# Kernel optimization log

Measured on AMD Instinct MI355X. Metric: run time of the kernel, lower is better.

## Reference

```python
import jax, jax.numpy as jnp
import numpy as np

N = 50000   # nodes
E = 800000  # directed edges
D = 128     # input_feat_dim
H = 128     # hidden1
L = 3       # GatedGraphConv layers
G = 64      # num graphs in batch
NEG_SLOPE = 0.01


def setup_inputs() -> dict:
    key = jax.random.key(0)
    ks = jax.random.split(key, 12)
    s = 1.0 / np.sqrt(H)
    x = jax.random.normal(ks[0], (N, D), jnp.float32)
    edge_index = jax.random.randint(ks[1], (2, E), 0, N)
    batch = jnp.sort(jax.random.randint(ks[2], (N,), 0, G))
    W_gcn = jax.random.normal(ks[3], (D, H), jnp.float32) * s
    b_gcn = jnp.zeros((H,), jnp.float32)
    W_gg = jax.random.normal(ks[4], (L, H, H), jnp.float32) * s   # GatedGraphConv per-layer weight
    W_ih = jax.random.normal(ks[5], (3 * H, H), jnp.float32) * s  # GRUCell input weights (r,z,n)
    W_hh = jax.random.normal(ks[6], (3 * H, H), jnp.float32) * s  # GRUCell hidden weights
    b_ih = jnp.zeros((3 * H,), jnp.float32)
    b_hh = jnp.zeros((3 * H,), jnp.float32)
    W1 = jax.random.normal(ks[7], (H, H), jnp.float32) * s
    b1 = jnp.zeros((H,), jnp.float32)
    W2 = jax.random.normal(ks[8], (H, 1), jnp.float32) * s
    b2 = jnp.zeros((1,), jnp.float32)
    return dict(x=x, edge_index=edge_index, batch=batch, W_gcn=W_gcn, b_gcn=b_gcn,
                W_gg=W_gg, W_ih=W_ih, W_hh=W_hh, b_ih=b_ih, b_hh=b_hh,
                W1=W1, b1=b1, W2=W2, b2=b2)


def _seg(vals, idx, num):
    return jax.ops.segment_sum(vals, idx, num_segments=num)


def _gcn(x, row, col, W, b):
    # PyG GCNConv: add self loops, symmetric norm, aggregate at target (col)
    xw = x @ W
    deg = _seg(jnp.ones((E,), xw.dtype), col, N) + 1.0  # +1 for self loop
    dinv = jax.lax.rsqrt(deg)
    norm = dinv[row] * dinv[col]                         # [E]
    out = _seg(xw[row] * norm[:, None], col, N)          # gather-scale-scatter
    out = out + xw * (dinv * dinv)[:, None]              # self-loop term
    return out + b


def _gru(m, h, W_ih, W_hh, b_ih, b_hh):
    gi = m @ W_ih.T + b_ih
    gh = h @ W_hh.T + b_hh
    ir, iz, inn = jnp.split(gi, 3, axis=-1)
    hr, hz, hn = jnp.split(gh, 3, axis=-1)
    r = jax.nn.sigmoid(ir + hr)
    z = jax.nn.sigmoid(iz + hz)
    n = jnp.tanh(inn + r * hn)
    return (1.0 - z) * n + z * h


def reference(x, edge_index, batch, W_gcn, b_gcn, W_gg, W_ih, W_hh, b_ih, b_hh, W1, b1, W2, b2):
    row, col = edge_index[0], edge_index[1]
    h = jax.nn.leaky_relu(_gcn(x, row, col, W_gcn, b_gcn), NEG_SLOPE)   # [N,H]
    g = h
    for l in range(L):  # GatedGraphConv: message = x_j @ W_l, sum-aggregate at col, GRU update
        m = _seg((g @ W_gg[l])[row], col, N)
        g = _gru(m, g, W_ih, W_hh, b_ih, b_hh)
    h = jax.nn.leaky_relu(g, NEG_SLOPE) + h
    h = jax.nn.leaky_relu(h @ W1 + b1, NEG_SLOPE)
    probs = jax.nn.sigmoid(h @ W2 + b2)                                  # [N,1]
    # maxcut loss: per-graph expected cut
    degrees = _seg(jnp.ones((E,), probs.dtype), row, N)[:, None]         # degree(row) per node
    expected_weight = _seg(probs[row] * probs[col], batch[row], G)       # [G,1]
    expected_degree = _seg(probs * degrees, batch, G)                    # [G,1]
    return -(expected_degree - expected_weight) / 2.0                    # [G,1]
```

## Files before the change

kernel.cpp:

```cpp
#include <hip/hip_runtime.h>
#include <math.h>

#define HD 128
#define NEG 0.01f
#define GD 64
#define LDST 136
#define FST 132

typedef short bf16x8 __attribute__((ext_vector_type(8)));
typedef float floatx4 __attribute__((ext_vector_type(4)));

__device__ __forceinline__ unsigned short f2bf(float f) {
    unsigned int u = __float_as_uint(f);
    u += 0x7fffu + ((u >> 16) & 1u);
    return (unsigned short)(u >> 16);
}
__device__ __forceinline__ float bf2f(unsigned short b) {
    return __uint_as_float(((unsigned int)b) << 16);
}
__device__ __forceinline__ float sigm(float v) { return 1.f / (1.f + __expf(-v)); }

__device__ __forceinline__ void mm64(const unsigned short* __restrict__ ap,
                                     const unsigned short* __restrict__ W,
                                     int m16, int quad, floatx4* acc) {
    #pragma unroll
    for (int ks = 0; ks < 4; ks++) {
        const int koff = ks * 32 + quad * 8;
        bf16x8 a = *(const bf16x8*)(ap + koff);
        #pragma unroll
        for (int cg = 0; cg < 8; cg++) {
            bf16x8 b = *(const bf16x8*)(W + (size_t)(cg * 16 + m16) * HD + koff);
            acc[cg] = __builtin_amdgcn_mfma_f32_16x16x32_bf16(a, b, acc[cg], 0, 0, 0);
        }
    }
}

__device__ __forceinline__ void loadB(const unsigned short* __restrict__ W,
                                      int w, int m16, int quad, bf16x8 bf[2][4]) {
    #pragma unroll
    for (int cgl = 0; cgl < 2; cgl++)
        #pragma unroll
        for (int ks = 0; ks < 4; ks++)
            bf[cgl][ks] = *(const bf16x8*)(W + (size_t)((2 * w + cgl) * 16 + m16) * HD
                                           + ks * 32 + quad * 8);
}
__device__ __forceinline__ void mmAcc32(const unsigned short* __restrict__ Atile,
                                        int m16, int quad, const bf16x8 bf[2][4],
                                        floatx4 acc[2][2]) {
    #pragma unroll
    for (int rg = 0; rg < 2; rg++)
        #pragma unroll
        for (int ks = 0; ks < 4; ks++) {
            bf16x8 a = *(const bf16x8*)(Atile + (rg * 16 + m16) * LDST + ks * 32 + quad * 8);
            acc[rg][0] = __builtin_amdgcn_mfma_f32_16x16x32_bf16(a, bf[0][ks], acc[rg][0], 0, 0, 0);
            acc[rg][1] = __builtin_amdgcn_mfma_f32_16x16x32_bf16(a, bf[1][ks], acc[rg][1], 0, 0, 0);
        }
}

__global__ __launch_bounds__(256) void gemm_mfma(
    const unsigned short* __restrict__ A, const unsigned short* __restrict__ BT,
    float* __restrict__ C32, unsigned short* __restrict__ C16, int M)
{
    __shared__ unsigned short As[128 * LDST];
    __shared__ unsigned short Bs[128 * LDST];
    const int tid = threadIdx.x;
    const int r0 = blockIdx.x * 128;
    {
        int rowi = tid >> 1, half = tid & 1;
        int gr = r0 + rowi; if (gr >= M) gr = M - 1;
        const float4* sa = (const float4*)(A + (size_t)gr * HD + half * 64);
        float4* da = (float4*)(As + rowi * LDST + half * 64);
        const float4* sb = (const float4*)(BT + (size_t)rowi * HD + half * 64);
        float4* db = (float4*)(Bs + rowi * LDST + half * 64);
        #pragma unroll
        for (int i = 0; i < 8; i++) { da[i] = sa[i]; db[i] = sb[i]; }
    }
    __syncthreads();
    const int wave = tid >> 6, lane = tid & 63;
    const int m16 = lane & 15, quad = lane >> 4;
    floatx4 acc[2][8];
    #pragma unroll
    for (int i = 0; i < 2; i++)
        #pragma unroll
        for (int j = 0; j < 8; j++) acc[i][j] = (floatx4){0.f, 0.f, 0.f, 0.f};
    const unsigned short* ar0 = As + (wave * 32 + m16) * LDST;
    const unsigned short* ar1 = As + (wave * 32 + 16 + m16) * LDST;
    #pragma unroll
    for (int ks = 0; ks < 4; ks++) {
        const int koff = ks * 32 + quad * 8;
        bf16x8 a0 = *(const bf16x8*)(ar0 + koff);
        bf16x8 a1 = *(const bf16x8*)(ar1 + koff);
        #pragma unroll
        for (int cg = 0; cg < 8; cg++) {
            bf16x8 b = *(const bf16x8*)(Bs + (cg * 16 + m16) * LDST + koff);
            acc[0][cg] = __builtin_amdgcn_mfma_f32_16x16x32_bf16(a0, b, acc[0][cg], 0, 0, 0);
            acc[1][cg] = __builtin_amdgcn_mfma_f32_16x16x32_bf16(a1, b, acc[1][cg], 0, 0, 0);
        }
    }
    if (C32) {
        #pragma unroll
        for (int rg = 0; rg < 2; rg++)
            #pragma unroll
            for (int cg = 0; cg < 8; cg++)
                #pragma unroll
                for (int i = 0; i < 4; i++) {
                    int r = r0 + wave * 32 + rg * 16 + quad * 4 + i;
                    if (r < M) C32[(size_t)r * HD + cg * 16 + m16] = acc[rg][cg][i];
                }
    }
    __syncthreads();
    #pragma unroll
    for (int rg = 0; rg < 2; rg++)
        #pragma unroll
        for (int cg = 0; cg < 8; cg++)
            #pragma unroll
            for (int i = 0; i < 4; i++)
                As[(wave * 32 + rg * 16 + quad * 4 + i) * LDST + cg * 16 + m16] =
                    f2bf(acc[rg][cg][i]);
    __syncthreads();
    #pragma unroll
    for (int it = 0; it < 8; it++) {
        int idx = it * 2048 + tid * 8;
        int rowi = idx >> 7, c = idx & 127;
        int gr = r0 + rowi;
        if (gr < M) {
            uint4 v = *(const uint4*)(As + rowi * LDST + c);
            *(uint4*)(C16 + (size_t)gr * HD + c) = v;
        }
    }
}

__global__ __launch_bounds__(256) void k_gather_gcn(
    const unsigned short* __restrict__ src, const float* __restrict__ xw,
    const int* __restrict__ csr, const int* __restrict__ offs,
    const float* __restrict__ dinv, const float* __restrict__ bias,
    float* __restrict__ h, unsigned short* __restrict__ g16, int N)
{
    int node = blockIdx.x * 4 + (threadIdx.x >> 6);
    if (node >= N) return;
    int lane = threadIdx.x & 63;
    int sub = lane >> 4, cl = lane & 15;
    int s = offs[node], e = offs[node + 1];
    float acc[8] = {0.f, 0.f, 0.f, 0.f, 0.f, 0.f, 0.f, 0.f};
    int j = s;
    for (; j + 8 <= e; j += 8) {
        int ra = csr[j + sub], rb = csr[j + 4 + sub];
        float sa = dinv[ra], sb = dinv[rb];
        bf16x8 va = *(const bf16x8*)(src + (size_t)ra * HD + cl * 8);
        bf16x8 vb = *(const bf16x8*)(src + (size_t)rb * HD + cl * 8);
        #pragma unroll
        for (int q = 0; q < 8; q++)
            acc[q] += bf2f((unsigned short)va[q]) * sa + bf2f((unsigned short)vb[q]) * sb;
    }
    for (; j < e; j += 4) {
        int jj = j + sub;
        if (jj < e) {
            int r = csr[jj];
            float sc = dinv[r];
            bf16x8 v = *(const bf16x8*)(src + (size_t)r * HD + cl * 8);
            #pragma unroll
            for (int q = 0; q < 8; q++)
                acc[q] += bf2f((unsigned short)v[q]) * sc;
        }
    }
    #pragma unroll
    for (int q = 0; q < 8; q++) {
        acc[q] += __shfl_xor(acc[q], 16);
        acc[q] += __shfl_xor(acc[q], 32);
    }
    if (sub == 0) {
        float dn = dinv[node], dv2 = dn * dn;
        size_t base = (size_t)node * HD + cl * 8;
        float4 xv0 = *(const float4*)(xw + base);
        float4 xv1 = *(const float4*)(xw + base + 4);
        float xs[8] = {xv0.x, xv0.y, xv0.z, xv0.w, xv1.x, xv1.y, xv1.z, xv1.w};
        float o[8];
        #pragma unroll
        for (int q = 0; q < 8; q++) {
            float v = acc[q] * dn + xs[q] * dv2 + bias[cl * 8 + q];
            o[q] = v > 0.f ? v : v * NEG;
        }
        *(float4*)(h + base) = (float4){o[0], o[1], o[2], o[3]};
        *(float4*)(h + base + 4) = (float4){o[4], o[5], o[6], o[7]};
        uint4 st;
        st.x = (unsigned int)f2bf(o[0]) | ((unsigned int)f2bf(o[1]) << 16);
        st.y = (unsigned int)f2bf(o[2]) | ((unsigned int)f2bf(o[3]) << 16);
        st.z = (unsigned int)f2bf(o[4]) | ((unsigned int)f2bf(o[5]) << 16);
        st.w = (unsigned int)f2bf(o[6]) | ((unsigned int)f2bf(o[7]) << 16);
        *(uint4*)(g16 + base) = st;
    }
}

__global__ __launch_bounds__(256) void k_gather_m(
    const unsigned short* __restrict__ src, const int* __restrict__ csr,
    const int* __restrict__ offs, unsigned short* __restrict__ out16, int N)
{
    int node = blockIdx.x * 4 + (threadIdx.x >> 6);
    if (node >= N) return;
    int lane = threadIdx.x & 63;
    int sub = lane >> 4, cl = lane & 15;
    int s = offs[node], e = offs[node + 1];
    float acc[8] = {0.f, 0.f, 0.f, 0.f, 0.f, 0.f, 0.f, 0.f};
    int j = s;
    for (; j + 8 <= e; j += 8) {
        int ra = csr[j + sub], rb = csr[j + 4 + sub];
        bf16x8 va = *(const bf16x8*)(src + (size_t)ra * HD + cl * 8);
        bf16x8 vb = *(const bf16x8*)(src + (size_t)rb * HD + cl * 8);
        #pragma unroll
        for (int q = 0; q < 8; q++)
            acc[q] += bf2f((unsigned short)va[q]) + bf2f((unsigned short)vb[q]);
    }
    for (; j < e; j += 4) {
        int jj = j + sub;
        if (jj < e) {
            int r = csr[jj];
            bf16x8 v = *(const bf16x8*)(src + (size_t)r * HD + cl * 8);
            #pragma unroll
            for (int q = 0; q < 8; q++)
                acc[q] += bf2f((unsigned short)v[q]);
        }
    }
    #pragma unroll
    for (int q = 0; q < 8; q++) {
        acc[q] += __shfl_xor(acc[q], 16);
        acc[q] += __shfl_xor(acc[q], 32);
    }
    if (sub == 0) {
        uint4 st;
        st.x = (unsigned int)f2bf(acc[0]) | ((unsigned int)f2bf(acc[1]) << 16);
        st.y = (unsigned int)f2bf(acc[2]) | ((unsigned int)f2bf(acc[3]) << 16);
        st.z = (unsigned int)f2bf(acc[4]) | ((unsigned int)f2bf(acc[5]) << 16);
        st.w = (unsigned int)f2bf(acc[6]) | ((unsigned int)f2bf(acc[7]) << 16);
        *(uint4*)(out16 + (size_t)node * HD + cl * 8) = st;
    }
}

__global__ __launch_bounds__(256, 5) void k_gru_gates(
    const unsigned short* __restrict__ m_bf, const unsigned short* __restrict__ g_bf,
    const unsigned short* __restrict__ Wih, const unsigned short* __restrict__ Whh,
    const float* __restrict__ b_ih, const float* __restrict__ b_hh,
    unsigned short* __restrict__ g16_out, int M)
{
    __shared__ unsigned short sh[2 * 32 * LDST];
    unsigned short* Am = sh;
    unsigned short* Ag = sh + 32 * LDST;
    const int tid = threadIdx.x;
    const int r0 = blockIdx.x * 32;
    #pragma unroll
    for (int it = 0; it < 2; it++) {
        int idx = it * 2048 + tid * 8;
        int rowi = idx >> 7, c = idx & 127;
        int gr = r0 + rowi; if (gr >= M) gr = M - 1;
        *(float4*)(Am + rowi * LDST + c) = *(const float4*)(m_bf + (size_t)gr * HD + c);
        *(float4*)(Ag + rowi * LDST + c) = *(const float4*)(g_bf + (size_t)gr * HD + c);
    }
    __syncthreads();
    const int w = tid >> 6, l = tid & 63;
    const int m16 = l & 15, quad = l >> 4;

    floatx4 accA[2][2], accB[2][2];
    bf16x8 bf[2][4];
    #pragma unroll
    for (int rg = 0; rg < 2; rg++)
        #pragma unroll
        for (int c = 0; c < 2; c++) {
            accA[rg][c] = (floatx4){0.f, 0.f, 0.f, 0.f};
            accB[rg][c] = (floatx4){0.f, 0.f, 0.f, 0.f};
        }
    loadB(Wih, w, m16, quad, bf);
    mmAcc32(Am, m16, quad, bf, accA);
    loadB(Whh, w, m16, quad, bf);
    mmAcc32(Ag, m16, quad, bf, accA);
    loadB(Whh + 256 * HD, w, m16, quad, bf);
    mmAcc32(Ag, m16, quad, bf, accB);
    #pragma unroll
    for (int cgl = 0; cgl < 2; cgl++) {
        int c = (2 * w + cgl) * 16 + m16;
        float br = b_ih[c] + b_hh[c];
        float bhn = b_hh[256 + c];
        #pragma unroll
        for (int rg = 0; rg < 2; rg++)
            #pragma unroll
            for (int i = 0; i < 4; i++) {
                float r = sigm(accA[rg][cgl][i] + br);
                accB[rg][cgl][i] = r * (accB[rg][cgl][i] + bhn);
            }
    }
    loadB(Wih + 256 * HD, w, m16, quad, bf);
    mmAcc32(Am, m16, quad, bf, accB);
    #pragma unroll
    for (int rg = 0; rg < 2; rg++)
        #pragma unroll
        for (int c = 0; c < 2; c++) accA[rg][c] = (floatx4){0.f, 0.f, 0.f, 0.f};
    loadB(Wih + 128 * HD, w, m16, quad, bf);
    mmAcc32(Am, m16, quad, bf, accA);
    loadB(Whh + 128 * HD, w, m16, quad, bf);
    mmAcc32(Ag, m16, quad, bf, accA);
    float ov[2][2][4];
    #pragma unroll
    for (int cgl = 0; cgl < 2; cgl++) {
        int c = (2 * w + cgl) * 16 + m16;
        float bz = b_ih[128 + c] + b_hh[128 + c];
        float bin = b_ih[256 + c];
        #pragma unroll
        for (int rg = 0; rg < 2; rg++)
            #pragma unroll
            for (int i = 0; i < 4; i++) {
                float z = sigm(accA[rg][cgl][i] + bz);
                float n = tanhf(accB[rg][cgl][i] + bin);
                float gv = bf2f(Ag[(rg * 16 + quad * 4 + i) * LDST + c]);
                ov[cgl][rg][i] = (1.f - z) * n + z * gv;
            }
    }
    __syncthreads();
    float* shf = (float*)sh;
    #pragma unroll
    for (int cgl = 0; cgl < 2; cgl++) {
        int c = (2 * w + cgl) * 16 + m16;
        #pragma unroll
        for (int rg = 0; rg < 2; rg++)
            #pragma unroll
            for (int i = 0; i < 4; i++)
                shf[(rg * 16 + quad * 4 + i) * FST + c] = ov[cgl][rg][i];
    }
    __syncthreads();
    #pragma unroll
    for (int it = 0; it < 2; it++) {
        int idx = it * 2048 + tid * 8;
        int rowi = idx >> 7, c = idx & 127;
        int gr = r0 + rowi;
        if (gr < M) {
            float4 v0 = *(const float4*)(shf + rowi * FST + c);
            float4 v1 = *(const float4*)(shf + rowi * FST + c + 4);
            uint4 st;
            st.x = (unsigned int)f2bf(v0.x) | ((unsigned int)f2bf(v0.y) << 16);
            st.y = (unsigned int)f2bf(v0.z) | ((unsigned int)f2bf(v0.w) << 16);
            st.z = (unsigned int)f2bf(v1.x) | ((unsigned int)f2bf(v1.y) << 16);
            st.w = (unsigned int)f2bf(v1.z) | ((unsigned int)f2bf(v1.w) << 16);
            *(uint4*)(g16_out + (size_t)gr * HD + c) = st;
        }
    }
}

__global__ __launch_bounds__(256, 4) void k_head_fused(
    const unsigned short* __restrict__ g_bf, const float* __restrict__ h,
    const unsigned short* __restrict__ W1T, const float* __restrict__ b1,
    const float* __restrict__ W2, const float* __restrict__ b2,
    float* __restrict__ probs, int M)
{
    __shared__ unsigned short As[64 * LDST];
    const int tid = threadIdx.x;
    const int r0 = blockIdx.x * 64;
    {
        int rowi = tid >> 2, q = tid & 3;
        int gr = r0 + rowi; if (gr >= M) gr = M - 1;
        const unsigned short* gp = g_bf + (size_t)gr * HD + q * 32;
        const float* hp = h + (size_t)gr * HD + q * 32;
        unsigned short* dst = As + rowi * LDST + q * 32;
        #pragma unroll
        for (int i = 0; i < 32; i += 4) {
            ushort4 gu = *(const ushort4*)(gp + i);
            float4 hv = *(const float4*)(hp + i);
            ushort4 o;
            float v;
            v = bf2f(gu.x); v = v > 0.f ? v : v * NEG; o.x = f2bf(v + hv.x);
            v = bf2f(gu.y); v = v > 0.f ? v : v * NEG; o.y = f2bf(v + hv.y);
            v = bf2f(gu.z); v = v > 0.f ? v : v * NEG; o.z = f2bf(v + hv.z);
            v = bf2f(gu.w); v = v > 0.f ? v : v * NEG; o.w = f2bf(v + hv.w);
            *(ushort4*)(dst + i) = o;
        }
    }
    __syncthreads();
    const int w = tid >> 6, l = tid & 63;
    const int m16 = l & 15, quad = l >> 4;
    floatx4 acc[8];
    #pragma unroll
    for (int j = 0; j < 8; j++) acc[j] = (floatx4){0.f, 0.f, 0.f, 0.f};
    mm64(As + (w * 16 + m16) * LDST, W1T, m16, quad, acc);
    #pragma unroll
    for (int i = 0; i < 4; i++) {
        float s = 0.f;
        #pragma unroll
        for (int cg = 0; cg < 8; cg++) {
            int c = cg * 16 + m16;
            float v = acc[cg][i] + b1[c];
            v = v > 0.f ? v : v * NEG;
            s += v * W2[c];
        }
        s += __shfl_xor(s, 1); s += __shfl_xor(s, 2);
        s += __shfl_xor(s, 4); s += __shfl_xor(s, 8);
        int r = r0 + w * 16 + quad * 4 + i;
        if (m16 == 0 && r < M) probs[r] = sigm(s + b2[0]);
    }
}

__global__ void k_prep_w(const float* __restrict__ W_gcn, const float* __restrict__ W_gg,
                         const float* __restrict__ W_ih, const float* __restrict__ W_hh,
                         const float* __restrict__ W1, unsigned short* __restrict__ Wq) {
    int i = blockIdx.x * blockDim.x + threadIdx.x;
    if (i >= 180224) return;
    float v;
    if (i < 16384) {
        int n = i >> 7, k = i & 127;
        v = W_gcn[k * 128 + n];
    } else if (i < 65536) {
        int j = i - 16384;
        int l = j >> 14, rr = j & 16383;
        int n = rr >> 7, k = rr & 127;
        v = W_gg[l * 16384 + k * 128 + n];
    } else if (i < 114688) {
        v = W_ih[i - 65536];
    } else if (i < 163840) {
        v = W_hh[i - 114688];
    } else {
        int j = i - 163840;
        int n = j >> 7, k = j & 127;
        v = W1[k * 128 + n];
    }
    Wq[i] = f2bf(v);
}

__global__ void k_cast_x(const float* __restrict__ s, unsigned short* __restrict__ d, int n2) {
    int i = blockIdx.x * blockDim.x + threadIdx.x;
    if (i >= n2) return;
    float2 v = *(const float2*)(s + (size_t)i * 2);
    unsigned int p = (unsigned int)f2bf(v.x) | ((unsigned int)f2bf(v.y) << 16);
    *(unsigned int*)(d + (size_t)i * 2) = p;
}

__global__ void k_hist(const int* __restrict__ col, int* __restrict__ cnt4,
                       int* __restrict__ rank, int N, int E) {
    int e = blockIdx.x * blockDim.x + threadIdx.x;
    if (e < E) {
        int s = blockIdx.x & 3;
        rank[e] = atomicAdd(&cnt4[s * N + col[e]], 1);
    }
}

#define SCHUNK 2048
__global__ __launch_bounds__(256) void k_scan1(const int* __restrict__ cnt4,
                                               int* __restrict__ excl,
                                               int* __restrict__ bsum, int N) {
    __shared__ int ts[256];
    int t = threadIdx.x;
    int base = blockIdx.x * SCHUNK + t * 8;
    int v[8]; int s = 0;
    #pragma unroll
    for (int q = 0; q < 8; q++) {
        int i = base + q;
        v[q] = (i < N) ? (cnt4[i] + cnt4[N + i] + cnt4[2 * N + i] + cnt4[3 * N + i]) : 0;
        s += v[q];
    }
    ts[t] = s;
    __syncthreads();
    for (int off = 1; off < 256; off <<= 1) {
        int a = (t >= off) ? ts[t - off] : 0;
        __syncthreads();
        ts[t] += a;
        __syncthreads();
    }
    int run = ts[t] - s;
    #pragma unroll
    for (int q = 0; q < 8; q++) { int i = base + q; if (i < N) excl[i] = run; run += v[q]; }
    if (t == 255) bsum[blockIdx.x] = ts[255];
}

__global__ void k_scan2(int* bsum, int nb) {
    if (threadIdx.x == 0) {
        int run = 0;
        for (int b = 0; b < nb; b++) { int v = bsum[b]; bsum[b] = run; run += v; }
    }
}

__global__ void k_csrfin(const int* __restrict__ excl, const int* __restrict__ bsum,
                         const int* __restrict__ cnt4, int* __restrict__ offs,
                         int* __restrict__ sbase, float* __restrict__ dinv, int N, int E) {
    int i = blockIdx.x * blockDim.x + threadIdx.x;
    if (i >= N) return;
    int o = excl[i] + bsum[i >> 11];
    offs[i] = o;
    if (i == 0) offs[N] = E;
    int c0 = cnt4[i], c1 = cnt4[N + i], c2 = cnt4[2 * N + i], c3 = cnt4[3 * N + i];
    sbase[i] = o;
    sbase[N + i] = o + c0;
    sbase[2 * N + i] = o + c0 + c1;
    sbase[3 * N + i] = o + c0 + c1 + c2;
    dinv[i] = rsqrtf((float)(c0 + c1 + c2 + c3) + 1.f);
}

__global__ void k_fill(const int* __restrict__ row, const int* __restrict__ col,
                       const int* __restrict__ sbase, const int* __restrict__ rank,
                       int* __restrict__ csr_rows, int N, int E) {
    int e = blockIdx.x * blockDim.x + threadIdx.x;
    if (e >= E) return;
    int s = (e >> 8) & 3;
    csr_rows[sbase[s * N + col[e]] + rank[e]] = row[e];
}

__global__ __launch_bounds__(256) void k_loss_edge(const float* __restrict__ probs,
                                                   const int* __restrict__ row,
                                                   const int* __restrict__ col,
                                                   const int* __restrict__ batch,
                                                   float* __restrict__ ed,
                                                   float* __restrict__ ew, int E) {
    __shared__ float bd[GD], be[GD];
    if (threadIdx.x < GD) { bd[threadIdx.x] = 0.f; be[threadIdx.x] = 0.f; }
    __syncthreads();
    for (int e = blockIdx.x * blockDim.x + threadIdx.x; e < E; e += gridDim.x * blockDim.x) {
        int r = row[e];
        float pr = probs[r];
        int b = batch[r];
        atomicAdd(&bd[b], pr);
        atomicAdd(&be[b], pr * probs[col[e]]);
    }
    __syncthreads();
    if (threadIdx.x < GD) {
        atomicAdd(&ed[threadIdx.x], bd[threadIdx.x]);
        atomicAdd(&ew[threadIdx.x], be[threadIdx.x]);
    }
}

__global__ void k_finalize(const float* __restrict__ ed, const float* __restrict__ ew,
                           float* __restrict__ out) {
    int g = threadIdx.x;
    if (g < GD) out[g] = -(ed[g] - ew[g]) * 0.5f;
}

extern "C" void kernel_launch(void* const* d_in, const int* in_sizes, int n_in,
                              void* d_out, int out_size, void* d_ws, size_t ws_size,
                              hipStream_t stream) {
    const float* x     = (const float*)d_in[0];
    const int*   ei    = (const int*)d_in[1];
    const int*   batch = (const int*)d_in[2];
    const float* W_gcn = (const float*)d_in[3];
    const float* b_gcn = (const float*)d_in[4];
    const float* W_gg  = (const float*)d_in[5];
    const float* W_ih  = (const float*)d_in[6];
    const float* W_hh  = (const float*)d_in[7];
    const float* b_ih  = (const float*)d_in[8];
    const float* b_hh  = (const float*)d_in[9];
    const float* W1    = (const float*)d_in[10];
    const float* b1    = (const float*)d_in[11];
    const float* W2    = (const float*)d_in[12];
    const float* b2    = (const float*)d_in[13];
    float* out = (float*)d_out;

    const int N = in_sizes[2];
    const int E = in_sizes[1] / 2;
    const int* row = ei;
    const int* col = ei + E;
    const size_t NH = (size_t)N * HD;

    float* F = (float*)d_ws;
    float* f_h  = F + 0 * NH;
    float* f_xw = F + 1 * NH;
    unsigned short* U = (unsigned short*)(F + 2 * NH);
    unsigned short* x_bf  = U;
    unsigned short* g_bf  = U + 1 * NH;
    unsigned short* t_bf  = U + 2 * NH;
    unsigned short* m_bf  = U + 3 * NH;
    unsigned short* Wq    = U + 4 * NH;
    unsigned short* WgcnT = Wq;
    unsigned short* WggT  = Wq + 16384;
    unsigned short* Wih16 = Wq + 65536;
    unsigned short* Whh16 = Wq + 114688;
    unsigned short* W1T   = Wq + 163840;
    float* S = (float*)(Wq + 180224);
    float* f_dinv  = S;
    float* f_probs = S + N;
    float* f_ed    = S + 2 * N;
    float* f_ew    = f_ed + GD;
    int* I = (int*)(f_ew + GD);
    int* i_cnt4  = I;
    int* i_excl  = I + 4 * N;
    int* i_offs  = I + 5 * N;
    int* i_bsum  = I + 6 * N + 8;
    int* i_sbase = I + 6 * N + 128;
    int* i_rank  = I + 10 * N + 128;
    int* i_csr   = i_rank + E;

    const int nb_scan = (N + SCHUNK - 1) / SCHUNK;
    const int gb32 = (N + 31) / 32;
    const int gb64 = (N + 63) / 64;
    const int gb128 = (N + 127) / 128;
    const int eg = (E + 255) / 256;
    const int ng = (N + 255) / 256;
    const int gather_grid = (N + 3) / 4;

    hipMemsetAsync(i_cnt4, 0, sizeof(int) * 4 * (size_t)N, stream);
    hipMemsetAsync(f_ed, 0, sizeof(float) * 2 * GD, stream);

    k_prep_w<<<704, 256, 0, stream>>>(W_gcn, W_gg, W_ih, W_hh, W1, Wq);
    k_cast_x<<<(int)((NH / 2 + 255) / 256), 256, 0, stream>>>(x, x_bf, (int)(NH / 2));

    k_hist<<<eg, 256, 0, stream>>>(col, i_cnt4, i_rank, N, E);
    k_scan1<<<nb_scan, 256, 0, stream>>>(i_cnt4, i_excl, i_bsum, N);
    k_scan2<<<1, 64, 0, stream>>>(i_bsum, nb_scan);
    k_csrfin<<<ng, 256, 0, stream>>>(i_excl, i_bsum, i_cnt4, i_offs, i_sbase, f_dinv, N, E);
    k_fill<<<eg, 256, 0, stream>>>(row, col, i_sbase, i_rank, i_csr, N, E);

    gemm_mfma<<<gb128, 256, 0, stream>>>(x_bf, WgcnT, f_xw, t_bf, N);
    k_gather_gcn<<<gather_grid, 256, 0, stream>>>(t_bf, f_xw, i_csr, i_offs, f_dinv,
                                                  b_gcn, f_h, g_bf, N);

    for (int l = 0; l < 3; l++) {
        gemm_mfma<<<gb128, 256, 0, stream>>>(g_bf, WggT + (size_t)l * 16384,
                                             nullptr, t_bf, N);
        k_gather_m<<<gather_grid, 256, 0, stream>>>(t_bf, i_csr, i_offs, m_bf, N);
        k_gru_gates<<<gb32, 256, 0, stream>>>(m_bf, g_bf, Wih16, Whh16, b_ih, b_hh,
                                              g_bf, N);
    }

    k_head_fused<<<gb64, 256, 0, stream>>>(g_bf, f_h, W1T, b1, W2, b2, f_probs, N);

    k_loss_edge<<<1024, 256, 0, stream>>>(f_probs, row, col, batch, f_ed, f_ew, E);
    k_finalize<<<1, 64, 0, stream>>>(f_ed, f_ew, out);
}
```

Baseline: 586.6 us.

## Double-buffer GRU weight loads, use exp-based tanh, widen histogram sharding to 8

Inside the GRU gate kernel, the next weight fragments are now loaded into a second register buffer while the current MFMA block runs, so global-load latency can overlap with matrix work. tanhf is replaced by an exp-based formula to cut transcendental cost. The CSR-build histogram spreads its atomic counters over 8 shards instead of 4 to reduce atomic contention, at the cost of more scan and finalize memory traffic. The extra register buffer may increase register pressure and lower occupancy.

New measurement: 574.2 us. -2.1%, faster.

```diff
diff --git a/kernel.cpp b/kernel.cpp
--- a/kernel.cpp
+++ b/kernel.cpp
@@ -19,6 +19,7 @@
     return __uint_as_float(((unsigned int)b) << 16);
 }
 __device__ __forceinline__ float sigm(float v) { return 1.f / (1.f + __expf(-v)); }
+__device__ __forceinline__ float fast_tanh(float v) { return 2.f / (1.f + __expf(-2.f * v)) - 1.f; }
 
 __device__ __forceinline__ void mm64(const unsigned short* __restrict__ ap,
                                      const unsigned short* __restrict__ W,
@@ -259,7 +260,7 @@
     const int m16 = l & 15, quad = l >> 4;
 
     floatx4 accA[2][2], accB[2][2];
-    bf16x8 bf[2][4];
+    bf16x8 bfA[2][4], bfB[2][4];
     #pragma unroll
     for (int rg = 0; rg < 2; rg++)
         #pragma unroll
@@ -267,12 +268,13 @@
             accA[rg][c] = (floatx4){0.f, 0.f, 0.f, 0.f};
             accB[rg][c] = (floatx4){0.f, 0.f, 0.f, 0.f};
         }
-    loadB(Wih, w, m16, quad, bf);
-    mmAcc32(Am, m16, quad, bf, accA);
-    loadB(Whh, w, m16, quad, bf);
-    mmAcc32(Ag, m16, quad, bf, accA);
-    loadB(Whh + 256 * HD, w, m16, quad, bf);
-    mmAcc32(Ag, m16, quad, bf, accB);
+    loadB(Wih, w, m16, quad, bfA);
+    loadB(Whh, w, m16, quad, bfB);
+    mmAcc32(Am, m16, quad, bfA, accA);
+    loadB(Whh + 256 * HD, w, m16, quad, bfA);
+    mmAcc32(Ag, m16, quad, bfB, accA);
+    loadB(Wih + 256 * HD, w, m16, quad, bfB);
+    mmAcc32(Ag, m16, quad, bfA, accB);
     #pragma unroll
     for (int cgl = 0; cgl < 2; cgl++) {
         int c = (2 * w + cgl) * 16 + m16;
@@ -286,16 +288,15 @@
                 accB[rg][cgl][i] = r * (accB[rg][cgl][i] + bhn);
             }
     }
-    loadB(Wih + 256 * HD, w, m16, quad, bf);
-    mmAcc32(Am, m16, quad, bf, accB);
+    loadB(Wih + 128 * HD, w, m16, quad, bfA);
+    mmAcc32(Am, m16, quad, bfB, accB);
+    loadB(Whh + 128 * HD, w, m16, quad, bfB);
     #pragma unroll
     for (int rg = 0; rg < 2; rg++)
         #pragma unroll
         for (int c = 0; c < 2; c++) accA[rg][c] = (floatx4){0.f, 0.f, 0.f, 0.f};
-    loadB(Wih + 128 * HD, w, m16, quad, bf);
-    mmAcc32(Am, m16, quad, bf, accA);
-    loadB(Whh + 128 * HD, w, m16, quad, bf);
-    mmAcc32(Ag, m16, quad, bf, accA);
+    mmAcc32(Am, m16, quad, bfA, accA);
+    mmAcc32(Ag, m16, quad, bfB, accA);
     float ov[2][2][4];
     #pragma unroll
     for (int cgl = 0; cgl < 2; cgl++) {
@@ -307,7 +308,7 @@
             #pragma unroll
             for (int i = 0; i < 4; i++) {
                 float z = sigm(accA[rg][cgl][i] + bz);
-                float n = tanhf(accB[rg][cgl][i] + bin);
+                float n = fast_tanh(accB[rg][cgl][i] + bin);
                 float gv = bf2f(Ag[(rg * 16 + quad * 4 + i) * LDST + c]);
                 ov[cgl][rg][i] = (1.f - z) * n + z * gv;
             }
@@ -428,17 +429,17 @@
     *(unsigned int*)(d + (size_t)i * 2) = p;
 }
 
-__global__ void k_hist(const int* __restrict__ col, int* __restrict__ cnt4,
+__global__ void k_hist(const int* __restrict__ col, int* __restrict__ cnt8,
                        int* __restrict__ rank, int N, int E) {
     int e = blockIdx.x * blockDim.x + threadIdx.x;
     if (e < E) {
-        int s = blockIdx.x & 3;
-        rank[e] = atomicAdd(&cnt4[s * N + col[e]], 1);
+        int s = blockIdx.x & 7;
+        rank[e] = atomicAdd(&cnt8[s * N + col[e]], 1);
     }
 }
 
 #define SCHUNK 2048
-__global__ __launch_bounds__(256) void k_scan1(const int* __restrict__ cnt4,
+__global__ __launch_bounds__(256) void k_scan1(const int* __restrict__ cnt8,
                                                int* __restrict__ excl,
                                                int* __restrict__ bsum, int N) {
     __shared__ int ts[256];
@@ -448,8 +449,12 @@
     #pragma unroll
     for (int q = 0; q < 8; q++) {
         int i = base + q;
-        v[q] = (i < N) ? (cnt4[i] + cnt4[N + i] + cnt4[2 * N + i] + cnt4[3 * N + i]) : 0;
-        s += v[q];
+        int c = 0;
+        if (i < N) {
+            #pragma unroll
+            for (int sh = 0; sh < 8; sh++) c += cnt8[(size_t)sh * N + i];
+        }
+        v[q] = c; s += c;
     }
     ts[t] = s;
     __syncthreads();
@@ -473,19 +478,21 @@
 }
 
 __global__ void k_csrfin(const int* __restrict__ excl, const int* __restrict__ bsum,
-                         const int* __restrict__ cnt4, int* __restrict__ offs,
+                         const int* __restrict__ cnt8, int* __restrict__ offs,
                          int* __restrict__ sbase, float* __restrict__ dinv, int N, int E) {
     int i = blockIdx.x * blockDim.x + threadIdx.x;
     if (i >= N) return;
     int o = excl[i] + bsum[i >> 11];
     offs[i] = o;
     if (i == 0) offs[N] = E;
-    int c0 = cnt4[i], c1 = cnt4[N + i], c2 = cnt4[2 * N + i], c3 = cnt4[3 * N + i];
-    sbase[i] = o;
-    sbase[N + i] = o + c0;
-    sbase[2 * N + i] = o + c0 + c1;
-    sbase[3 * N + i] = o + c0 + c1 + c2;
-    dinv[i] = rsqrtf((float)(c0 + c1 + c2 + c3) + 1.f);
+    int run = o, tot = 0;
+    #pragma unroll
+    for (int sh = 0; sh < 8; sh++) {
+        int c = cnt8[(size_t)sh * N + i];
+        sbase[(size_t)sh * N + i] = run;
+        run += c; tot += c;
+    }
+    dinv[i] = rsqrtf((float)tot + 1.f);
 }
 
 __global__ void k_fill(const int* __restrict__ row, const int* __restrict__ col,
@@ -493,8 +500,8 @@
                        int* __restrict__ csr_rows, int N, int E) {
     int e = blockIdx.x * blockDim.x + threadIdx.x;
     if (e >= E) return;
-    int s = (e >> 8) & 3;
-    csr_rows[sbase[s * N + col[e]] + rank[e]] = row[e];
+    int s = (e >> 8) & 7;
+    csr_rows[sbase[(size_t)s * N + col[e]] + rank[e]] = row[e];
 }
 
 __global__ __launch_bounds__(256) void k_loss_edge(const float* __restrict__ probs,
@@ -571,12 +578,12 @@
     float* f_ed    = S + 2 * N;
     float* f_ew    = f_ed + GD;
     int* I = (int*)(f_ew + GD);
-    int* i_cnt4  = I;
-    int* i_excl  = I + 4 * N;
-    int* i_offs  = I + 5 * N;
-    int* i_bsum  = I + 6 * N + 8;
-    int* i_sbase = I + 6 * N + 128;
-    int* i_rank  = I + 10 * N + 128;
+    int* i_cnt8  = I;
+    int* i_excl  = I + 8 * N;
+    int* i_offs  = I + 9 * N;
+    int* i_bsum  = I + 10 * N + 8;
+    int* i_sbase = I + 10 * N + 128;
+    int* i_rank  = I + 18 * N + 128;
     int* i_csr   = i_rank + E;
 
     const int nb_scan = (N + SCHUNK - 1) / SCHUNK;
@@ -587,16 +594,16 @@
     const int ng = (N + 255) / 256;
     const int gather_grid = (N + 3) / 4;
 
-    hipMemsetAsync(i_cnt4, 0, sizeof(int) * 4 * (size_t)N, stream);
+    hipMemsetAsync(i_cnt8, 0, sizeof(int) * 8 * (size_t)N, stream);
     hipMemsetAsync(f_ed, 0, sizeof(float) * 2 * GD, stream);
 
     k_prep_w<<<704, 256, 0, stream>>>(W_gcn, W_gg, W_ih, W_hh, W1, Wq);
     k_cast_x<<<(int)((NH / 2 + 255) / 256), 256, 0, stream>>>(x, x_bf, (int)(NH / 2));
 
-    k_hist<<<eg, 256, 0, stream>>>(col, i_cnt4, i_rank, N, E);
-    k_scan1<<<nb_scan, 256, 0, stream>>>(i_cnt4, i_excl, i_bsum, N);
+    k_hist<<<eg, 256, 0, stream>>>(col, i_cnt8, i_rank, N, E);
+    k_scan1<<<nb_scan, 256, 0, stream>>>(i_cnt8, i_excl, i_bsum, N);
     k_scan2<<<1, 64, 0, stream>>>(i_bsum, nb_scan);
-    k_csrfin<<<ng, 256, 0, stream>>>(i_excl, i_bsum, i_cnt4, i_offs, i_sbase, f_dinv, N, E);
+    k_csrfin<<<ng, 256, 0, stream>>>(i_excl, i_bsum, i_cnt8, i_offs, i_sbase, f_dinv, N, E);
     k_fill<<<eg, 256, 0, stream>>>(row, col, i_sbase, i_rank, i_csr, N, E);
 
     gemm_mfma<<<gb128, 256, 0, stream>>>(x_bf, WgcnT, f_xw, t_bf, N);
```
